# Kernel optimization log

Hardware: AMD Instinct MI355X
Metric: run time of the kernel (lower is better)

## Reference

```python
import jax, jax.numpy as jnp
import numpy as np

N = 100000   # nodes
E = 1600000  # edges
IN, H, C = 128, 128, 40


def setup_inputs() -> dict:
    key = jax.random.key(0)
    ks = jax.random.split(key, 8)
    feat = jax.random.normal(ks[0], (N, IN), jnp.float32)
    src = jax.random.randint(ks[1], (E,), 0, N, jnp.int32)
    dst = jax.random.randint(ks[2], (E,), 0, N, jnp.int32)
    # Glorot-ish init like dgl GraphConv.reset_parameters
    W0 = jax.random.normal(ks[3], (IN, H), jnp.float32) * (1.0 / np.sqrt(IN))
    W1 = jax.random.normal(ks[4], (H, H), jnp.float32) * (1.0 / np.sqrt(H))
    W2 = jax.random.normal(ks[5], (H, C), jnp.float32) * (1.0 / np.sqrt(H))
    b0 = jnp.zeros((H,), jnp.float32)
    b1 = jnp.zeros((H,), jnp.float32)
    b2 = jnp.zeros((C,), jnp.float32)
    return {"feat": feat, "src": src, "dst": dst,
            "W0": W0, "b0": b0, "W1": W1, "b1": b1, "W2": W2, "b2": b2}


def _graph_conv(h, src, dst, W, b):
    # dgl GraphConv with norm='both': D_out^{-1/2} pre-scale, sum-aggregate,
    # D_in^{-1/2} post-scale; degrees clamped to min 1. Weight applied before
    # aggregation (in_feats >= out_feats path) -- math is identical either way.
    ones = jnp.ones((src.shape[0],), h.dtype)
    deg_out = jnp.maximum(jax.ops.segment_sum(ones, src, num_segments=N), 1.0)
    deg_in = jnp.maximum(jax.ops.segment_sum(ones, dst, num_segments=N), 1.0)
    h = h * (deg_out ** -0.5)[:, None]
    h = h @ W                                   # [N, out]
    agg = jax.ops.segment_sum(h[src], dst, num_segments=N)  # gather+scatter
    return agg * (deg_in ** -0.5)[:, None] + b


def reference(feat, src, dst, W0, b0, W1, b1, W2, b2):
    h = jax.nn.relu(_graph_conv(feat, src, dst, W0, b0))  # dropout p=0 -> identity
    h = jax.nn.relu(_graph_conv(h, src, dst, W1, b1))
    return _graph_conv(h, src, dst, W2, b2)
```

## Files before the change

### kernel.cpp

```cpp
#include <hip/hip_runtime.h>

#define NN 100000
#define EE 1600000
#define ELLW 64
#define NXCD 8
#define RNG ((NN + NXCD - 1) / NXCD)
#define GEMMN ((NN + 31) / 32)
#define BUILDN ((EE / 256) * NXCD)

__device__ __forceinline__ unsigned int pack_bf2(float a, float b) {
    unsigned int ua = __float_as_uint(a);
    ua += 0x7FFFu + ((ua >> 16) & 1u);
    unsigned int ub = __float_as_uint(b);
    ub += 0x7FFFu + ((ub >> 16) & 1u);
    return (ua >> 16) | (ub & 0xFFFF0000u);
}

__device__ __forceinline__ void nt_store_f2(float* p, float x, float y) {
    unsigned long long v = (unsigned long long)__float_as_uint(x) |
                           ((unsigned long long)__float_as_uint(y) << 32);
    __builtin_nontemporal_store(v, (unsigned long long*)p);
}

__device__ __forceinline__ void gemm128_body(const float* __restrict__ X, const int* __restrict__ dout,
                                             const float* __restrict__ W, unsigned int* __restrict__ Y,
                                             int n, int row0, int tid, float* Xs, int scaled) {
    const float4* X4 = (const float4*)X;
#pragma unroll
    for (int idx = tid; idx < 1024; idx += 256) {
        int r = idx & 31, c4 = idx >> 5;
        int row = row0 + r;
        float4 v = make_float4(0.f, 0.f, 0.f, 0.f);
        float s = 0.f;
        if (row < n) {
            v = X4[(size_t)row * 32 + c4];
            s = scaled ? rsqrtf((float)max(1, dout[row])) : 1.f;
        }
        Xs[(c4 * 4 + 0) * 32 + r] = v.x * s;
        Xs[(c4 * 4 + 1) * 32 + r] = v.y * s;
        Xs[(c4 * 4 + 2) * 32 + r] = v.z * s;
        Xs[(c4 * 4 + 3) * 32 + r] = v.w * s;
    }
    __syncthreads();
    int cg = tid & 31;
    int rg = tid >> 5;
    float a[4][4];
#pragma unroll
    for (int r = 0; r < 4; ++r)
#pragma unroll
        for (int c = 0; c < 4; ++c) a[r][c] = 0.f;
    const float4* W4 = (const float4*)W;
#pragma unroll 4
    for (int k = 0; k < 128; ++k) {
        float4 xv = *(const float4*)&Xs[k * 32 + rg * 4];
        float4 wv = W4[k * 32 + cg];
        float xr[4] = {xv.x, xv.y, xv.z, xv.w};
        float wc[4] = {wv.x, wv.y, wv.z, wv.w};
#pragma unroll
        for (int r = 0; r < 4; ++r)
#pragma unroll
            for (int c = 0; c < 4; ++c) a[r][c] = fmaf(xr[r], wc[c], a[r][c]);
    }
    int rbase = row0 + rg * 4;
    uint2* Y2 = (uint2*)Y;
#pragma unroll
    for (int r = 0; r < 4; ++r) {
        if (rbase + r < n) {
            Y2[(size_t)(rbase + r) * 32 + cg] =
                make_uint2(pack_bf2(a[r][0], a[r][1]), pack_bf2(a[r][2], a[r][3]));
        }
    }
}

__global__ __launch_bounds__(256) void k_build_gemm0(const int* __restrict__ src, const int* __restrict__ dst,
                                                     int* __restrict__ din, int* __restrict__ dout,
                                                     int* __restrict__ ell,
                                                     const float* __restrict__ X, const float* __restrict__ W,
                                                     unsigned int* __restrict__ Y) {
    __shared__ float Xs[128 * 32];
    int tid = threadIdx.x;
    int q = blockIdx.x / 17, rem = blockIdx.x % 17;
    if (rem == 16) {
        gemm128_body(X, nullptr, W, Y, NN, q * 32, tid, Xs, 0);
        return;
    }
    int idx = q * 16 + rem;
    int r = idx & (NXCD - 1);
    int slice = idx >> 3;
    int i = slice * 256 + tid;
    if (i >= EE) return;
    int s = __builtin_nontemporal_load(&src[i]);
    int d = __builtin_nontemporal_load(&dst[i]);
    int lo = r * RNG, hi = lo + RNG;
    if (d >= lo && d < hi) {
        int p = atomicAdd(&din[d], 1);
        if (p < ELLW) ell[(size_t)d * ELLW + p] = s;
    }
    if (s >= lo && s < hi) {
        atomicAdd(&dout[s], 1);
    }
}

__global__ __launch_bounds__(256) void k_gemm128(const float* __restrict__ X, const int* __restrict__ dout,
                                                 const float* __restrict__ W, unsigned int* __restrict__ Y, int n) {
    __shared__ float Xs[128 * 32];
    gemm128_body(X, dout, W, Y, n, blockIdx.x * 32, threadIdx.x, Xs, 1);
}

__global__ __launch_bounds__(320) void k_gemm40(const float* __restrict__ X, const int* __restrict__ dout,
                                                const float* __restrict__ W, unsigned int* __restrict__ Y, int n) {
    __shared__ float Xs[128 * 64];
    int tid = threadIdx.x;
    int row0 = blockIdx.x * 64;
    const float4* X4 = (const float4*)X;
    for (int idx = tid; idx < 2048; idx += 320) {
        int r = idx & 63, c4 = idx >> 6;
        int row = row0 + r;
        float4 v = make_float4(0.f, 0.f, 0.f, 0.f);
        float s = 0.f;
        if (row < n) { v = X4[(size_t)row * 32 + c4]; s = rsqrtf((float)max(1, dout[row])); }
        Xs[(c4 * 4 + 0) * 64 + r] = v.x * s;
        Xs[(c4 * 4 + 1) * 64 + r] = v.y * s;
        Xs[(c4 * 4 + 2) * 64 + r] = v.z * s;
        Xs[(c4 * 4 + 3) * 64 + r] = v.w * s;
    }
    __syncthreads();
    int cg = tid % 20;
    int rg = tid / 20;
    float a0x=0,a0y=0, a1x=0,a1y=0, a2x=0,a2y=0, a3x=0,a3y=0;
    const float2* W2 = (const float2*)W;
#pragma unroll 4
    for (int k = 0; k < 128; ++k) {
        float4 xv = *(const float4*)&Xs[k * 64 + rg * 4];
        float2 wv = W2[k * 20 + cg];
        a0x += xv.x * wv.x; a0y += xv.x * wv.y;
        a1x += xv.y * wv.x; a1y += xv.y * wv.y;
        a2x += xv.z * wv.x; a2y += xv.z * wv.y;
        a3x += xv.w * wv.x; a3y += xv.w * wv.y;
    }
    int rbase = row0 + rg * 4;
    if (rbase + 0 < n) Y[(size_t)(rbase + 0) * 32 + cg] = pack_bf2(a0x, a0y);
    if (rbase + 1 < n) Y[(size_t)(rbase + 1) * 32 + cg] = pack_bf2(a1x, a1y);
    if (rbase + 2 < n) Y[(size_t)(rbase + 2) * 32 + cg] = pack_bf2(a2x, a2y);
    if (rbase + 3 < n) Y[(size_t)(rbase + 3) * 32 + cg] = pack_bf2(a3x, a3y);
}

__global__ __launch_bounds__(256) void k_gather128(const unsigned int* __restrict__ h, const int* __restrict__ din,
                                                   const int* __restrict__ dout, const int* __restrict__ ell,
                                                   const float* __restrict__ b, float* __restrict__ out,
                                                   int n, int do_relu, int so_mode) {
    int wv = threadIdx.x >> 6, lane = threadIdx.x & 63;
    int v = blockIdx.x * 4 + wv;
    if (v >= n) return;
    int dv = din[v];
    int cnt = min(dv, ELLW);
    int cl = ell[(size_t)v * ELLW + lane];
    int cls = (lane < cnt) ? cl : 0;
    float scl = 1.f;
    if (so_mode) scl = rsqrtf((float)max(1, dout[cls]));
    float sx = 0.f, sy = 0.f;
    for (int j = 0; j < cnt; j += 8) {
        int cc[8]; float mk[8]; unsigned int t[8];
#pragma unroll
        for (int k = 0; k < 8; ++k) {
            int jj = j + k;
            int jc = jj < cnt ? jj : cnt - 1;
            cc[k] = __shfl(cls, jc);
            float sw = __shfl(scl, jc);
            mk[k] = (jj < cnt) ? sw : 0.f;
        }
#pragma unroll
        for (int k = 0; k < 8; ++k)
            t[k] = h[(size_t)cc[k] * 64 + lane];
#pragma unroll
        for (int k = 0; k < 8; ++k) {
            float x = __uint_as_float(t[k] << 16);
            float y = __uint_as_float(t[k] & 0xFFFF0000u);
            sx = fmaf(mk[k], x, sx);
            sy = fmaf(mk[k], y, sy);
        }
    }
    float sc = rsqrtf((float)max(1, dv));
    float2 bb = ((const float2*)b)[lane];
    float ox = sx * sc + bb.x;
    float oy = sy * sc + bb.y;
    if (do_relu) { ox = fmaxf(ox, 0.f); oy = fmaxf(oy, 0.f); }
    nt_store_f2((float*)((float2*)out + (size_t)v * 64 + lane), ox, oy);
}

__global__ __launch_bounds__(256) void k_gather40(const unsigned short* __restrict__ h, const int* __restrict__ din,
                                                  const int* __restrict__ ell,
                                                  const float* __restrict__ b, float* __restrict__ out, int n) {
    int wv = threadIdx.x >> 6, lane = threadIdx.x & 63;
    int v = blockIdx.x * 4 + wv;
    if (v >= n) return;
    int dv = din[v];
    int cnt = min(dv, ELLW);
    int cl = ell[(size_t)v * ELLW + lane];
    int cls = (lane < cnt) ? cl : 0;
    float s = 0.f;
    for (int j = 0; j < cnt; j += 8) {
        int cc[8]; float mk[8]; unsigned short t[8];
#pragma unroll
        for (int k = 0; k < 8; ++k) {
            int jj = j + k;
            cc[k] = __shfl(cls, jj < cnt ? jj : cnt - 1);
            mk[k] = (jj < cnt) ? 1.f : 0.f;
        }
        if (lane < 40) {
#pragma unroll
            for (int k = 0; k < 8; ++k) t[k] = h[(size_t)cc[k] * 64 + lane];
#pragma unroll
            for (int k = 0; k < 8; ++k)
                s = fmaf(mk[k], __uint_as_float((unsigned int)t[k] << 16), s);
        }
    }
    if (lane < 40) {
        out[(size_t)v * 40 + lane] = s * rsqrtf((float)max(1, dv)) + b[lane];
    }
}

extern "C" void kernel_launch(void* const* d_in, const int* in_sizes, int n_in,
                              void* d_out, int out_size, void* d_ws, size_t ws_size,
                              hipStream_t stream) {
    const float* feat = (const float*)d_in[0];
    const int*   src  = (const int*)d_in[1];
    const int*   dst  = (const int*)d_in[2];
    const float* W0   = (const float*)d_in[3];
    const float* b0   = (const float*)d_in[4];
    const float* W1   = (const float*)d_in[5];
    const float* b1   = (const float*)d_in[6];
    const float* W2   = (const float*)d_in[7];
    const float* b2   = (const float*)d_in[8];
    float* out = (float*)d_out;

    char* w = (char*)d_ws;
    int*   din       = (int*)w;    w += (size_t)NN * 4;
    int*   dout      = (int*)w;    w += (size_t)NN * 4;
    int*   ell       = (int*)w;    w += (size_t)NN * ELLW * 4;
    unsigned int* h2 = (unsigned int*)w; w += (size_t)NN * 128 * 2;
    unsigned int* h40 = (unsigned int*)w; w += (size_t)NN * 32 * 4;
    float* agg       = (float*)w;  w += (size_t)NN * 128 * 4;

    hipMemsetAsync(d_ws, 0, (size_t)NN * 8, stream);

    int gath_grid = (NN + 3) / 4;

    k_build_gemm0<<<GEMMN * 17, 256, 0, stream>>>(src, dst, din, dout, ell, feat, W0, h2);
    k_gather128<<<gath_grid, 256, 0, stream>>>(h2, din, dout, ell, b0, agg, NN, 1, 1);
    k_gemm128<<<GEMMN, 256, 0, stream>>>(agg, dout, W1, h2, NN);
    k_gather128<<<gath_grid, 256, 0, stream>>>(h2, din, dout, ell, b1, agg, NN, 1, 0);
    k_gemm40<<<(NN + 63) / 64, 320, 0, stream>>>(agg, dout, W2, h40, NN);
    k_gather40<<<gath_grid, 256, 0, stream>>>((const unsigned short*)h40, din, ell, b2, out, NN);
}
```

Before: 567.5 us.

## Fuse gather with following GEMM and vectorize edge build without XCD partitioning

Merges each 128-wide gather/aggregate with the next layer's GEMM in one kernel. Aggregated rows are staged in shared memory, so the fp32 intermediate no longer goes through global memory, and the kernel count drops from six to four. The edge build now reads src/dst as int4 vectors and does all atomics in one pass instead of filtering by XCD range, and the gemm bodies drop row bounds checks because NN is a multiple of 32. The cost is lower parallelism in the gather (8 nodes per wave, serially) and atomics that may contend across XCDs.

New measurement: 553.2 us. 1.03x faster.

```diff
diff --git a/kernel.cpp b/kernel.cpp
--- a/kernel.cpp
+++ b/kernel.cpp
@@ -3,10 +3,11 @@
 #define NN 100000
 #define EE 1600000
 #define ELLW 64
-#define NXCD 8
-#define RNG ((NN + NXCD - 1) / NXCD)
 #define GEMMN ((NN + 31) / 32)
-#define BUILDN ((EE / 256) * NXCD)
+#define BQ ((EE / 4 + 511) / 512)
+#define GRID_BG (BQ * 5)
+
+typedef int iv4 __attribute__((ext_vector_type(4)));
 
 __device__ __forceinline__ unsigned int pack_bf2(float a, float b) {
     unsigned int ua = __float_as_uint(a);
@@ -16,30 +17,19 @@
     return (ua >> 16) | (ub & 0xFFFF0000u);
 }
 
-__device__ __forceinline__ void nt_store_f2(float* p, float x, float y) {
-    unsigned long long v = (unsigned long long)__float_as_uint(x) |
-                           ((unsigned long long)__float_as_uint(y) << 32);
-    __builtin_nontemporal_store(v, (unsigned long long*)p);
-}
-
-__device__ __forceinline__ void gemm128_body(const float* __restrict__ X, const int* __restrict__ dout,
+__device__ __forceinline__ void gemm128_body(const float* __restrict__ X,
                                              const float* __restrict__ W, unsigned int* __restrict__ Y,
-                                             int n, int row0, int tid, float* Xs, int scaled) {
+                                             int row0, int tid, float* Xs) {
     const float4* X4 = (const float4*)X;
 #pragma unroll
     for (int idx = tid; idx < 1024; idx += 256) {
         int r = idx & 31, c4 = idx >> 5;
         int row = row0 + r;
-        float4 v = make_float4(0.f, 0.f, 0.f, 0.f);
-        float s = 0.f;
-        if (row < n) {
-            v = X4[(size_t)row * 32 + c4];
-            s = scaled ? rsqrtf((float)max(1, dout[row])) : 1.f;
-        }
-        Xs[(c4 * 4 + 0) * 32 + r] = v.x * s;
-        Xs[(c4 * 4 + 1) * 32 + r] = v.y * s;
-        Xs[(c4 * 4 + 2) * 32 + r] = v.z * s;
-        Xs[(c4 * 4 + 3) * 32 + r] = v.w * s;
+        float4 v = X4[(size_t)row * 32 + c4];
+        Xs[(c4 * 4 + 0) * 32 + r] = v.x;
+        Xs[(c4 * 4 + 1) * 32 + r] = v.y;
+        Xs[(c4 * 4 + 2) * 32 + r] = v.z;
+        Xs[(c4 * 4 + 3) * 32 + r] = v.w;
     }
     __syncthreads();
     int cg = tid & 31;
@@ -65,10 +55,8 @@
     uint2* Y2 = (uint2*)Y;
 #pragma unroll
     for (int r = 0; r < 4; ++r) {
-        if (rbase + r < n) {
-            Y2[(size_t)(rbase + r) * 32 + cg] =
-                make_uint2(pack_bf2(a[r][0], a[r][1]), pack_bf2(a[r][2], a[r][3]));
-        }
+        Y2[(size_t)(rbase + r) * 32 + cg] =
+            make_uint2(pack_bf2(a[r][0], a[r][1]), pack_bf2(a[r][2], a[r][3]));
     }
 }
 
@@ -79,113 +67,171 @@
                                                      unsigned int* __restrict__ Y) {
     __shared__ float Xs[128 * 32];
     int tid = threadIdx.x;
-    int q = blockIdx.x / 17, rem = blockIdx.x % 17;
-    if (rem == 16) {
-        gemm128_body(X, nullptr, W, Y, NN, q * 32, tid, Xs, 0);
+    int q = blockIdx.x / 5, rem = blockIdx.x % 5;
+    if (rem) {
+        int g = q * 4 + (rem - 1);
+        if (g < GEMMN) gemm128_body(X, W, Y, g * 32, tid, Xs);
         return;
     }
-    int idx = q * 16 + rem;
-    int r = idx & (NXCD - 1);
-    int slice = idx >> 3;
-    int i = slice * 256 + tid;
-    if (i >= EE) return;
-    int s = __builtin_nontemporal_load(&src[i]);
-    int d = __builtin_nontemporal_load(&dst[i]);
-    int lo = r * RNG, hi = lo + RNG;
-    if (d >= lo && d < hi) {
-        int p = atomicAdd(&din[d], 1);
-        if (p < ELLW) ell[(size_t)d * ELLW + p] = s;
-    }
-    if (s >= lo && s < hi) {
-        atomicAdd(&dout[s], 1);
-    }
-}
-
-__global__ __launch_bounds__(256) void k_gemm128(const float* __restrict__ X, const int* __restrict__ dout,
-                                                 const float* __restrict__ W, unsigned int* __restrict__ Y, int n) {
-    __shared__ float Xs[128 * 32];
-    gemm128_body(X, dout, W, Y, n, blockIdx.x * 32, threadIdx.x, Xs, 1);
-}
-
-__global__ __launch_bounds__(320) void k_gemm40(const float* __restrict__ X, const int* __restrict__ dout,
-                                                const float* __restrict__ W, unsigned int* __restrict__ Y, int n) {
-    __shared__ float Xs[128 * 64];
+    const iv4* s4p = (const iv4*)src;
+    const iv4* d4p = (const iv4*)dst;
+    const int n4 = EE / 4;
+#pragma unroll
+    for (int h = 0; h < 2; ++h) {
+        int i4 = q * 512 + h * 256 + tid;
+        if (i4 < n4) {
+            iv4 s4 = __builtin_nontemporal_load(&s4p[i4]);
+            iv4 d4 = __builtin_nontemporal_load(&d4p[i4]);
+            int ss[4] = {s4.x, s4.y, s4.z, s4.w};
+            int dd[4] = {d4.x, d4.y, d4.z, d4.w};
+#pragma unroll
+            for (int k = 0; k < 4; ++k) {
+                int p = atomicAdd(&din[dd[k]], 1);
+                if (p < ELLW) ell[(size_t)dd[k] * ELLW + p] = ss[k];
+            }
+#pragma unroll
+            for (int k = 0; k < 4; ++k) atomicAdd(&dout[ss[k]], 1);
+        }
+    }
+}
+
+__global__ __launch_bounds__(256) void k_gathergemm128(const unsigned int* __restrict__ h,
+                                                       const int* __restrict__ din, const int* __restrict__ dout,
+                                                       const int* __restrict__ ell,
+                                                       const float* __restrict__ bias,
+                                                       const float* __restrict__ W,
+                                                       unsigned int* __restrict__ Y, int so_mode) {
+    __shared__ float Xs[128 * 36];
     int tid = threadIdx.x;
-    int row0 = blockIdx.x * 64;
-    const float4* X4 = (const float4*)X;
-    for (int idx = tid; idx < 2048; idx += 320) {
-        int r = idx & 63, c4 = idx >> 6;
-        int row = row0 + r;
-        float4 v = make_float4(0.f, 0.f, 0.f, 0.f);
-        float s = 0.f;
-        if (row < n) { v = X4[(size_t)row * 32 + c4]; s = rsqrtf((float)max(1, dout[row])); }
-        Xs[(c4 * 4 + 0) * 64 + r] = v.x * s;
-        Xs[(c4 * 4 + 1) * 64 + r] = v.y * s;
-        Xs[(c4 * 4 + 2) * 64 + r] = v.z * s;
-        Xs[(c4 * 4 + 3) * 64 + r] = v.w * s;
-    }
-    __syncthreads();
-    int cg = tid % 20;
-    int rg = tid / 20;
-    float a0x=0,a0y=0, a1x=0,a1y=0, a2x=0,a2y=0, a3x=0,a3y=0;
-    const float2* W2 = (const float2*)W;
+    int wv = tid >> 6, lane = tid & 63;
+    int row0 = blockIdx.x * 32;
+    float2 bb = ((const float2*)bias)[lane];
+    for (int j8 = 0; j8 < 8; ++j8) {
+        int r = wv * 8 + j8;
+        int v = row0 + r;
+        int dv = din[v];
+        int cnt = min(dv, ELLW);
+        int cl = ell[(size_t)v * ELLW + lane];
+        int cls = (lane < cnt) ? cl : 0;
+        float scl = 1.f;
+        if (so_mode) scl = rsqrtf((float)max(1, dout[cls]));
+        float sx = 0.f, sy = 0.f;
+        for (int j = 0; j < cnt; j += 8) {
+            int cc[8]; float mk[8]; unsigned int t[8];
+#pragma unroll
+            for (int k = 0; k < 8; ++k) {
+                int jj = j + k;
+                int jc = jj < cnt ? jj : cnt - 1;
+                cc[k] = __shfl(cls, jc);
+                float sw = so_mode ? __shfl(scl, jc) : 1.f;
+                mk[k] = (jj < cnt) ? sw : 0.f;
+            }
+#pragma unroll
+            for (int k = 0; k < 8; ++k) t[k] = h[(size_t)cc[k] * 64 + lane];
+#pragma unroll
+            for (int k = 0; k < 8; ++k) {
+                float x = __uint_as_float(t[k] << 16);
+                float y = __uint_as_float(t[k] & 0xFFFF0000u);
+                sx = fmaf(mk[k], x, sx);
+                sy = fmaf(mk[k], y, sy);
+            }
+        }
+        float si = rsqrtf((float)max(1, dv));
+        float so = rsqrtf((float)max(1, dout[v]));
+        float ox = fmaxf(sx * si + bb.x, 0.f) * so;
+        float oy = fmaxf(sy * si + bb.y, 0.f) * so;
+        Xs[(2 * lane) * 36 + r] = ox;
+        Xs[(2 * lane + 1) * 36 + r] = oy;
+    }
+    __syncthreads();
+    int cg = tid & 31, rg = tid >> 5;
+    float a[4][4];
+#pragma unroll
+    for (int r = 0; r < 4; ++r)
+#pragma unroll
+        for (int c = 0; c < 4; ++c) a[r][c] = 0.f;
+    const float4* W4 = (const float4*)W;
 #pragma unroll 4
     for (int k = 0; k < 128; ++k) {
-        float4 xv = *(const float4*)&Xs[k * 64 + rg * 4];
-        float2 wv = W2[k * 20 + cg];
-        a0x += xv.x * wv.x; a0y += xv.x * wv.y;
-        a1x += xv.y * wv.x; a1y += xv.y * wv.y;
-        a2x += xv.z * wv.x; a2y += xv.z * wv.y;
-        a3x += xv.w * wv.x; a3y += xv.w * wv.y;
+        float4 xv = *(const float4*)&Xs[k * 36 + rg * 4];
+        float4 wv4 = W4[k * 32 + cg];
+        float xr[4] = {xv.x, xv.y, xv.z, xv.w};
+        float wc[4] = {wv4.x, wv4.y, wv4.z, wv4.w};
+#pragma unroll
+        for (int r = 0; r < 4; ++r)
+#pragma unroll
+            for (int c = 0; c < 4; ++c) a[r][c] = fmaf(xr[r], wc[c], a[r][c]);
     }
     int rbase = row0 + rg * 4;
-    if (rbase + 0 < n) Y[(size_t)(rbase + 0) * 32 + cg] = pack_bf2(a0x, a0y);
-    if (rbase + 1 < n) Y[(size_t)(rbase + 1) * 32 + cg] = pack_bf2(a1x, a1y);
-    if (rbase + 2 < n) Y[(size_t)(rbase + 2) * 32 + cg] = pack_bf2(a2x, a2y);
-    if (rbase + 3 < n) Y[(size_t)(rbase + 3) * 32 + cg] = pack_bf2(a3x, a3y);
-}
-
-__global__ __launch_bounds__(256) void k_gather128(const unsigned int* __restrict__ h, const int* __restrict__ din,
-                                                   const int* __restrict__ dout, const int* __restrict__ ell,
-                                                   const float* __restrict__ b, float* __restrict__ out,
-                                                   int n, int do_relu, int so_mode) {
-    int wv = threadIdx.x >> 6, lane = threadIdx.x & 63;
-    int v = blockIdx.x * 4 + wv;
-    if (v >= n) return;
-    int dv = din[v];
-    int cnt = min(dv, ELLW);
-    int cl = ell[(size_t)v * ELLW + lane];
-    int cls = (lane < cnt) ? cl : 0;
-    float scl = 1.f;
-    if (so_mode) scl = rsqrtf((float)max(1, dout[cls]));
-    float sx = 0.f, sy = 0.f;
-    for (int j = 0; j < cnt; j += 8) {
-        int cc[8]; float mk[8]; unsigned int t[8];
-#pragma unroll
-        for (int k = 0; k < 8; ++k) {
-            int jj = j + k;
-            int jc = jj < cnt ? jj : cnt - 1;
-            cc[k] = __shfl(cls, jc);
-            float sw = __shfl(scl, jc);
-            mk[k] = (jj < cnt) ? sw : 0.f;
-        }
-#pragma unroll
-        for (int k = 0; k < 8; ++k)
-            t[k] = h[(size_t)cc[k] * 64 + lane];
-#pragma unroll
-        for (int k = 0; k < 8; ++k) {
-            float x = __uint_as_float(t[k] << 16);
-            float y = __uint_as_float(t[k] & 0xFFFF0000u);
-            sx = fmaf(mk[k], x, sx);
-            sy = fmaf(mk[k], y, sy);
-        }
-    }
-    float sc = rsqrtf((float)max(1, dv));
-    float2 bb = ((const float2*)b)[lane];
-    float ox = sx * sc + bb.x;
-    float oy = sy * sc + bb.y;
-    if (do_relu) { ox = fmaxf(ox, 0.f); oy = fmaxf(oy, 0.f); }
-    nt_store_f2((float*)((float2*)out + (size_t)v * 64 + lane), ox, oy);
+    uint2* Y2 = (uint2*)Y;
+#pragma unroll
+    for (int r = 0; r < 4; ++r) {
+        Y2[(size_t)(rbase + r) * 32 + cg] =
+            make_uint2(pack_bf2(a[r][0], a[r][1]), pack_bf2(a[r][2], a[r][3]));
+    }
+}
+
+__global__ __launch_bounds__(256) void k_gathergemm40(const unsigned int* __restrict__ h,
+                                                      const int* __restrict__ din, const int* __restrict__ dout,
+                                                      const int* __restrict__ ell,
+                                                      const float* __restrict__ bias,
+                                                      const float* __restrict__ W,
+                                                      unsigned int* __restrict__ Y) {
+    __shared__ float Xs[128 * 36];
+    __shared__ float Os[32 * 40];
+    int tid = threadIdx.x;
+    int wv = tid >> 6, lane = tid & 63;
+    int row0 = blockIdx.x * 32;
+    float2 bb = ((const float2*)bias)[lane];
+    for (int j8 = 0; j8 < 8; ++j8) {
+        int r = wv * 8 + j8;
+        int v = row0 + r;
+        int dv = din[v];
+        int cnt = min(dv, ELLW);
+        int cl = ell[(size_t)v * ELLW + lane];
+        int cls = (lane < cnt) ? cl : 0;
+        float sx = 0.f, sy = 0.f;
+        for (int j = 0; j < cnt; j += 8) {
+            int cc[8]; float mk[8]; unsigned int t[8];
+#pragma unroll
+            for (int k = 0; k < 8; ++k) {
+                int jj = j + k;
+                cc[k] = __shfl(cls, jj < cnt ? jj : cnt - 1);
+                mk[k] = (jj < cnt) ? 1.f : 0.f;
+            }
+#pragma unroll
+            for (int k = 0; k < 8; ++k) t[k] = h[(size_t)cc[k] * 64 + lane];
+#pragma unroll
+            for (int k = 0; k < 8; ++k) {
+                float x = __uint_as_float(t[k] << 16);
+                float y = __uint_as_float(t[k] & 0xFFFF0000u);
+                sx = fmaf(mk[k], x, sx);
+                sy = fmaf(mk[k], y, sy);
+            }
+        }
+        float si = rsqrtf((float)max(1, dv));
+        float so = rsqrtf((float)max(1, dout[v]));
+        float ox = fmaxf(sx * si + bb.x, 0.f) * so;
+        float oy = fmaxf(sy * si + bb.y, 0.f) * so;
+        Xs[(2 * lane) * 36 + r] = ox;
+        Xs[(2 * lane + 1) * 36 + r] = oy;
+    }
+    __syncthreads();
+    int rg = tid >> 3;
+    int cg = tid & 7;
+    float a[5] = {0.f, 0.f, 0.f, 0.f, 0.f};
+    for (int k = 0; k < 128; ++k) {
+        float x = Xs[k * 36 + rg];
+#pragma unroll
+        for (int c = 0; c < 5; ++c) a[c] = fmaf(x, W[k * 40 + cg * 5 + c], a[c]);
+    }
+#pragma unroll
+    for (int c = 0; c < 5; ++c) Os[rg * 40 + cg * 5 + c] = a[c];
+    __syncthreads();
+    for (int i = tid; i < 640; i += 256) {
+        int row = i / 20, pj = i % 20;
+        Y[(size_t)(row0 + row) * 32 + pj] = pack_bf2(Os[row * 40 + 2 * pj], Os[row * 40 + 2 * pj + 1]);
+    }
 }
 
 __global__ __launch_bounds__(256) void k_gather40(const unsigned short* __restrict__ h, const int* __restrict__ din,
@@ -239,17 +285,13 @@
     int*   dout      = (int*)w;    w += (size_t)NN * 4;
     int*   ell       = (int*)w;    w += (size_t)NN * ELLW * 4;
     unsigned int* h2 = (unsigned int*)w; w += (size_t)NN * 128 * 2;
+    unsigned int* h2b = (unsigned int*)w; w += (size_t)NN * 128 * 2;
     unsigned int* h40 = (unsigned int*)w; w += (size_t)NN * 32 * 4;
-    float* agg       = (float*)w;  w += (size_t)NN * 128 * 4;
-
-    hipMemsetAsync(d_ws, 0, (size_t)NN * 8, stream);
-
-    int gath_grid = (NN + 3) / 4;
-
-    k_build_gemm0<<<GEMMN * 17, 256, 0, stream>>>(src, dst, din, dout, ell, feat, W0, h2);
-    k_gather128<<<gath_grid, 256, 0, stream>>>(h2, din, dout, ell, b0, agg, NN, 1, 1);
-    k_gemm128<<<GEMMN, 256, 0, stream>>>(agg, dout, W1, h2, NN);
-    k_gather128<<<gath_grid, 256, 0, stream>>>(h2, din, dout, ell, b1, agg, NN, 1, 0);
-    k_gemm40<<<(NN + 63) / 64, 320, 0, stream>>>(agg, dout, W2, h40, NN);
-    k_gather40<<<gath_grid, 256, 0, stream>>>((const unsigned short*)h40, din, ell, b2, out, NN);
-}
+
+    (void)hipMemsetAsync(d_ws, 0, (size_t)NN * 8, stream);
+
+    k_build_gemm0<<<GRID_BG, 256, 0, stream>>>(src, dst, din, dout, ell, feat, W0, h2);
+    k_gathergemm128<<<GEMMN, 256, 0, stream>>>(h2, din, dout, ell, b0, W1, h2b, 1);
+    k_gathergemm40<<<GEMMN, 256, 0, stream>>>(h2b, din, dout, ell, b1, W2, h40);
+    k_gather40<<<(NN + 3) / 4, 256, 0, stream>>>((const unsigned short*)h40, din, ell, b2, out, NN);
+}
```
